# Performance work log

Hardware: AMD Instinct MI355X
Metric: run time of the kernel (lower is better)

Reference implementation:

```python
import jax, jax.numpy as jnp
import numpy as np

B, SQ, SK, D, DV = 8, 2048, 4096, 512, 256

def setup_inputs() -> dict:
    key = jax.random.key(0)
    k1, k2, k3, k4, k5 = jax.random.split(key, 5)
    X = jax.random.normal(k1, (B, SQ, D), dtype=jnp.float32)
    Y = jax.random.normal(k2, (SK, D), dtype=jnp.float32)
    Z = jax.random.normal(k3, (SK, D), dtype=jnp.float32)
    # Linear weights (torch stores [out, in]); scaled like default init
    W_k = jax.random.normal(k4, (D, D), dtype=jnp.float32) / np.sqrt(D)
    W_v = jax.random.normal(k5, (DV, D), dtype=jnp.float32) / np.sqrt(D)
    return {"X": X, "Y": Y, "Z": Z, "W_k": W_k, "W_v": W_v, "rate": 0}


def reference(X, Y, Z, W_k, W_v, rate):
    # key = W_k(Y).unsqueeze(0): [1, SK, D]; value = W_v(Z).unsqueeze(0): [1, SK, DV]
    key = (Y @ W_k.T)[None]
    value = (Z @ W_v.T)[None]
    # scores = X @ key^T / sqrt(d): [B, SQ, SK] (key batch dim broadcasts)
    scale = 1.0 / jnp.sqrt(jnp.asarray(X.shape[-1], dtype=X.dtype))
    scores = jnp.matmul(X, jnp.swapaxes(key, 1, 2)) * scale
    attn = jax.nn.softmax(scores, axis=-1)
    # dropout layers act as identity in eval mode
    out = jnp.matmul(attn, value)  # [B, SQ, DV]
    return out
```

## Files before the change

kernel.cpp:

```cpp
#include <hip/hip_runtime.h>
#include <hip/hip_bf16.h>

#define NB    8
#define SQN   2048
#define SKN   4096
#define DDIM  512
#define DVDIM 256
#define NROWS (NB*SQN)
#define NS    2
#define NJ    ((SKN/64)/NS)

typedef __attribute__((ext_vector_type(8))) short bf16x8;
typedef __attribute__((ext_vector_type(4))) short bf16x4;
typedef __attribute__((ext_vector_type(4))) float f32x4;

__device__ __forceinline__ short f2bf(float f) {
    unsigned u = __float_as_uint(f);
    return (short)((u + 0x7FFFu + ((u >> 16) & 1u)) >> 16);
}

__device__ __forceinline__ void gload_lds16(const void* g, void* l) {
    __builtin_amdgcn_global_load_lds(
        (const __attribute__((address_space(1))) unsigned int*)g,
        (__attribute__((address_space(3))) unsigned int*)l, 16, 0, 0);
}

__global__ __launch_bounds__(256, 2) void proj_gemms(
    const float* __restrict__ Y, const float* __restrict__ Z,
    const float* __restrict__ Wk, const float* __restrict__ Wv,
    unsigned short* __restrict__ keyb, unsigned short* __restrict__ vtb)
{
    __shared__ short sA[64*128];
    __shared__ short sB[64*128];
    const float *A, *Bm;
    unsigned short* C;
    int N, m0, n0;
    if (blockIdx.z == 0) {
        A = Y; Bm = Wk; C = keyb; N = DDIM;
        m0 = blockIdx.x * 64; n0 = blockIdx.y * 64;
    } else {
        int lin = blockIdx.x * 8 + blockIdx.y;
        if (lin >= 256) return;
        A = Wv; Bm = Z; C = vtb; N = SKN;
        m0 = (lin >> 6) * 64; n0 = (lin & 63) * 64;
    }
    const int tid  = threadIdx.x;
    const int wave = tid >> 6;
    const int lane = tid & 63;
    const int quad = lane >> 4;
    const int l15  = lane & 15;

    f32x4 acc[4];
    #pragma unroll
    for (int n = 0; n < 4; ++n) { acc[n][0]=0.f; acc[n][1]=0.f; acc[n][2]=0.f; acc[n][3]=0.f; }

    float4 ra[8], rb[8];
    #pragma unroll
    for (int it = 0; it < 8; ++it) {
        int f = it*1024 + tid*4, row = f >> 7, col = f & 127;
        ra[it] = *(const float4*)(A  + (size_t)(m0+row)*DDIM + col);
        rb[it] = *(const float4*)(Bm + (size_t)(n0+row)*DDIM + col);
    }

    for (int kc = 0; kc < DDIM; kc += 128) {
        __syncthreads();
        #pragma unroll
        for (int it = 0; it < 8; ++it) {
            int f = it*1024 + tid*4;
            bf16x4 a4; a4[0]=f2bf(ra[it].x); a4[1]=f2bf(ra[it].y); a4[2]=f2bf(ra[it].z); a4[3]=f2bf(ra[it].w);
            *(bf16x4*)(sA + f) = a4;
            bf16x4 b4; b4[0]=f2bf(rb[it].x); b4[1]=f2bf(rb[it].y); b4[2]=f2bf(rb[it].z); b4[3]=f2bf(rb[it].w);
            *(bf16x4*)(sB + f) = b4;
        }
        __syncthreads();
        if (kc + 128 < DDIM) {
            #pragma unroll
            for (int it = 0; it < 8; ++it) {
                int f = it*1024 + tid*4, row = f >> 7, col = f & 127;
                ra[it] = *(const float4*)(A  + (size_t)(m0+row)*DDIM + kc + 128 + col);
                rb[it] = *(const float4*)(Bm + (size_t)(n0+row)*DDIM + kc + 128 + col);
            }
        }
        #pragma unroll
        for (int t = 0; t < 4; ++t) {
            bf16x8 af = *(const bf16x8*)(sA + (wave*16 + l15)*128 + t*32 + quad*8);
            #pragma unroll
            for (int n = 0; n < 4; ++n) {
                bf16x8 bfr = *(const bf16x8*)(sB + (n*16 + l15)*128 + t*32 + quad*8);
                acc[n] = __builtin_amdgcn_mfma_f32_16x16x32_bf16(af, bfr, acc[n], 0, 0, 0);
            }
        }
    }
    #pragma unroll
    for (int n = 0; n < 4; ++n)
        #pragma unroll
        for (int r = 0; r < 4; ++r) {
            int m  = m0 + wave*16 + quad*4 + r;
            int nn = n0 + n*16 + l15;
            C[(size_t)m*N + nn] = (unsigned short)f2bf(acc[n][r]);
        }
}

__global__ __launch_bounds__(256, 2) void attn_fused(
    const float* __restrict__ X,
    const unsigned short* __restrict__ Kb,
    const unsigned short* __restrict__ Vt,
    float* __restrict__ Opart,
    float* __restrict__ Mpart,
    float* __restrict__ Lpart)
{
    __shared__ short sK[2][8192];
    __shared__ short sV[16384];
    __shared__ short sP[4096];
    const int tid  = threadIdx.x;
    const int wave = tid >> 6;
    const int lane = tid & 63;
    const int quad = lane >> 4;
    const int l15  = lane & 15;
    const int l7   = lane & 7;
    const int split = blockIdx.y;
    const int q0   = blockIdx.x * 64;
    const int sb0  = split * NJ;
    const float scale = 0.04419417382415922f;

    bf16x8 qf[16];
    {
        const float* xrow = X + (size_t)(q0 + wave*16 + l15) * DDIM;
        #pragma unroll
        for (int t = 0; t < 16; ++t) {
            float4 a = *(const float4*)(xrow + t*32 + quad*8);
            float4 b = *(const float4*)(xrow + t*32 + quad*8 + 4);
            bf16x8 q;
            q[0]=f2bf(a.x*scale); q[1]=f2bf(a.y*scale); q[2]=f2bf(a.z*scale); q[3]=f2bf(a.w*scale);
            q[4]=f2bf(b.x*scale); q[5]=f2bf(b.y*scale); q[6]=f2bf(b.z*scale); q[7]=f2bf(b.w*scale);
            qf[t] = q;
        }
    }

    f32x4 o[16];
    #pragma unroll
    for (int i = 0; i < 16; ++i) { o[i][0]=0.f; o[i][1]=0.f; o[i][2]=0.f; o[i][3]=0.f; }
    float m_r[4] = {-1e30f,-1e30f,-1e30f,-1e30f};
    float l_r[4] = {0.f,0.f,0.f,0.f};
    short* sPw = sP + wave*1024;

    const int wq   = wave*4 + quad;
    const int vrow = wave*8 + (lane>>3);
    const int vswz = (l7 ^ (lane>>3)) << 3;

    #define STAGE_K(sk0_, c_, buf_)                                            \
        do {                                                                   \
            const unsigned short* ksrc_ = Kb + (size_t)((sk0_) + wq)*DDIM      \
                + (c_)*128 + ((l15 ^ wq) << 3);                                \
            char* kdst_ = (char*)(buf_) + wave*1024;                           \
            _Pragma("unroll")                                                  \
            for (int it_ = 0; it_ < 4; ++it_)                                  \
                gload_lds16(ksrc_ + (size_t)it_*16*DDIM, kdst_ + it_*4096);    \
        } while (0)

    STAGE_K(sb0*64, 0, sK[0]);

    for (int j = 0; j < NJ; ++j) {
        const int sk0 = (sb0 + j) * 64;
        f32x4 s[4];
        #pragma unroll
        for (int n = 0; n < 4; ++n) { s[n][0]=0.f; s[n][1]=0.f; s[n][2]=0.f; s[n][3]=0.f; }

        #pragma unroll
        for (int c = 0; c < 4; ++c) {
            __syncthreads();
            if (c == 0) {
                const unsigned short* vsrc = Vt + sk0 + (size_t)vrow*SKN + vswz;
                char* vdst = (char*)sV + wave*1024;
                #pragma unroll
                for (int it = 0; it < 8; ++it)
                    gload_lds16(vsrc + (size_t)it*32*SKN, vdst + it*4096);
            }
            if (c < 3)            STAGE_K(sk0,      c + 1, sK[(c + 1) & 1]);
            else if (j + 1 < NJ)  STAGE_K(sk0 + 64, 0,     sK[0]);
            const short* sKc = sK[c & 1];
            #pragma unroll
            for (int t = 0; t < 4; ++t) {
                bf16x8 af = qf[c*4 + t];
                #pragma unroll
                for (int n = 0; n < 4; ++n) {
                    bf16x8 bfr = *(const bf16x8*)(sKc + (n*16 + l15)*128
                                                  + (((t*4 + quad) ^ l15) << 3));
                    s[n] = __builtin_amdgcn_mfma_f32_16x16x32_bf16(af, bfr, s[n], 0, 0, 0);
                }
            }
        }

        float alpha[4];
        int need_rescale = 0;
        #pragma unroll
        for (int r = 0; r < 4; ++r) {
            float v = fmaxf(fmaxf(s[0][r], s[1][r]), fmaxf(s[2][r], s[3][r]));
            v = fmaxf(v, __shfl_xor(v, 1));
            v = fmaxf(v, __shfl_xor(v, 2));
            v = fmaxf(v, __shfl_xor(v, 4));
            v = fmaxf(v, __shfl_xor(v, 8));
            float mn = fmaxf(m_r[r], v);
            float a  = __expf(m_r[r] - mn);
            alpha[r] = a;
            need_rescale |= (a < 1.0f);
            m_r[r] = mn;
            const int row = quad*4 + r;
            short* prow = sPw + row*64 + l7;
            const int rx = row & 7;
            float sum = 0.f;
            #pragma unroll
            for (int n = 0; n < 4; ++n) {
                float pv = __expf(s[n][r] - mn);
                sum += pv;
                prow[((n*2 + (l15 >> 3)) ^ rx) << 3] = f2bf(pv);
            }
            sum += __shfl_xor(sum, 1);
            sum += __shfl_xor(sum, 2);
            sum += __shfl_xor(sum, 4);
            sum += __shfl_xor(sum, 8);
            l_r[r] = l_r[r]*a + sum;
        }
        if (__any(need_rescale)) {
            #pragma unroll
            for (int n2 = 0; n2 < 16; ++n2)
                #pragma unroll
                for (int r = 0; r < 4; ++r) o[n2][r] *= alpha[r];
        }

        #pragma unroll
        for (int t2 = 0; t2 < 2; ++t2) {
            const int cx = (((t2*4 + quad) ^ l7) << 3);
            bf16x8 af = *(const bf16x8*)(sPw + l15*64 + cx);
            #pragma unroll
            for (int n2 = 0; n2 < 16; ++n2) {
                bf16x8 bfr = *(const bf16x8*)(sV + (n2*16 + l15)*64 + cx);
                o[n2] = __builtin_amdgcn_mfma_f32_16x16x32_bf16(af, bfr, o[n2], 0, 0, 0);
            }
        }
    }
    #undef STAGE_K

    const size_t base = (size_t)split * NROWS;
    #pragma unroll
    for (int r = 0; r < 4; ++r) {
        int row = q0 + wave*16 + quad*4 + r;
        if (l15 == 0) { Mpart[base + row] = m_r[r]; Lpart[base + row] = l_r[r]; }
        float* orow = Opart + (base + row) * (size_t)DVDIM;
        #pragma unroll
        for (int n2 = 0; n2 < 16; ++n2)
            orow[n2*16 + l15] = o[n2][r];
    }
}

__global__ void combine_splits(
    const float* __restrict__ Opart, const float* __restrict__ Mpart,
    const float* __restrict__ Lpart, float* __restrict__ out)
{
    const int row = blockIdx.x * 4 + (threadIdx.x >> 6);
    const int dv4 = (threadIdx.x & 63) * 4;
    float M = -1e30f;
    #pragma unroll
    for (int s = 0; s < NS; ++s) M = fmaxf(M, Mpart[(size_t)s*NROWS + row]);
    float denom = 0.f;
    float4 acc = make_float4(0.f, 0.f, 0.f, 0.f);
    #pragma unroll
    for (int s = 0; s < NS; ++s) {
        float w = __expf(Mpart[(size_t)s*NROWS + row] - M);
        denom += Lpart[(size_t)s*NROWS + row] * w;
        float4 ov = *(const float4*)(Opart + ((size_t)s*NROWS + row)*DVDIM + dv4);
        acc.x += ov.x*w; acc.y += ov.y*w; acc.z += ov.z*w; acc.w += ov.w*w;
    }
    float inv = 1.0f / denom;
    *(float4*)(out + (size_t)row*DVDIM + dv4)
        = make_float4(acc.x*inv, acc.y*inv, acc.z*inv, acc.w*inv);
}

extern "C" void kernel_launch(void* const* d_in, const int* in_sizes, int n_in,
                              void* d_out, int out_size, void* d_ws, size_t ws_size,
                              hipStream_t stream) {
    const float* X  = (const float*)d_in[0];
    const float* Y  = (const float*)d_in[1];
    const float* Z  = (const float*)d_in[2];
    const float* Wk = (const float*)d_in[3];
    const float* Wv = (const float*)d_in[4];
    float* out = (float*)d_out;

    char* ws = (char*)d_ws;
    unsigned short* keyb = (unsigned short*)ws;
    unsigned short* vtb  = (unsigned short*)(ws + (4u<<20));
    float* Opart = (float*)(ws + (6u<<20));
    float* Mpart = (float*)(ws + (6u<<20) + (size_t)NS*NROWS*DVDIM*4);
    float* Lpart = Mpart + (size_t)NS*NROWS;

    proj_gemms<<<dim3(64, 8, 2), dim3(256), 0, stream>>>(Y, Z, Wk, Wv, keyb, vtb);
    attn_fused<<<dim3(NROWS/64, NS), dim3(256), 0, stream>>>(
        X, keyb, vtb, Opart, Mpart, Lpart);
    combine_splits<<<dim3(NROWS/4), dim3(256), 0, stream>>>(Opart, Mpart, Lpart, out);
}
```

Baseline: 299.4 us.

## Fuse projections, attention and split combine into one persistent kernel with grid barrier

Merges the projection GEMMs, the split-K attention and the split combine into a single launch. The projection tiles are spread across all 512 blocks, then a global atomic barrier makes every block wait before attention starts. The split combine now runs in the second-arriving block of each pair, which reads its partner's partial results from a ticket and flag instead of a separate kernel. The change also drops the double-buffered K staging in favour of a single buffer with an extra barrier per chunk, and adds a memset launch. This trades launch gaps and one partial write/read for less K-load overlap and a grid-wide spin barrier that relies on all blocks being co-resident.

```diff
diff --git a/kernel.cpp b/kernel.cpp
--- a/kernel.cpp
+++ b/kernel.cpp
@@ -9,6 +9,7 @@
 #define NROWS (NB*SQN)
 #define NS    2
 #define NJ    ((SKN/64)/NS)
+#define NBLK  (256*NS)
 
 typedef __attribute__((ext_vector_type(8))) short bf16x8;
 typedef __attribute__((ext_vector_type(4))) short bf16x4;
@@ -25,103 +26,95 @@
         (__attribute__((address_space(3))) unsigned int*)l, 16, 0, 0);
 }
 
-__global__ __launch_bounds__(256, 2) void proj_gemms(
-    const float* __restrict__ Y, const float* __restrict__ Z,
-    const float* __restrict__ Wk, const float* __restrict__ Wv,
-    unsigned short* __restrict__ keyb, unsigned short* __restrict__ vtb)
-{
-    __shared__ short sA[64*128];
-    __shared__ short sB[64*128];
-    const float *A, *Bm;
-    unsigned short* C;
-    int N, m0, n0;
-    if (blockIdx.z == 0) {
-        A = Y; Bm = Wk; C = keyb; N = DDIM;
-        m0 = blockIdx.x * 64; n0 = blockIdx.y * 64;
-    } else {
-        int lin = blockIdx.x * 8 + blockIdx.y;
-        if (lin >= 256) return;
-        A = Wv; Bm = Z; C = vtb; N = SKN;
-        m0 = (lin >> 6) * 64; n0 = (lin & 63) * 64;
-    }
-    const int tid  = threadIdx.x;
-    const int wave = tid >> 6;
-    const int lane = tid & 63;
-    const int quad = lane >> 4;
-    const int l15  = lane & 15;
-
-    f32x4 acc[4];
-    #pragma unroll
-    for (int n = 0; n < 4; ++n) { acc[n][0]=0.f; acc[n][1]=0.f; acc[n][2]=0.f; acc[n][3]=0.f; }
-
-    float4 ra[8], rb[8];
-    #pragma unroll
-    for (int it = 0; it < 8; ++it) {
-        int f = it*1024 + tid*4, row = f >> 7, col = f & 127;
-        ra[it] = *(const float4*)(A  + (size_t)(m0+row)*DDIM + col);
-        rb[it] = *(const float4*)(Bm + (size_t)(n0+row)*DDIM + col);
-    }
-
-    for (int kc = 0; kc < DDIM; kc += 128) {
-        __syncthreads();
-        #pragma unroll
-        for (int it = 0; it < 8; ++it) {
-            int f = it*1024 + tid*4;
-            bf16x4 a4; a4[0]=f2bf(ra[it].x); a4[1]=f2bf(ra[it].y); a4[2]=f2bf(ra[it].z); a4[3]=f2bf(ra[it].w);
-            *(bf16x4*)(sA + f) = a4;
-            bf16x4 b4; b4[0]=f2bf(rb[it].x); b4[1]=f2bf(rb[it].y); b4[2]=f2bf(rb[it].z); b4[3]=f2bf(rb[it].w);
-            *(bf16x4*)(sB + f) = b4;
-        }
-        __syncthreads();
-        if (kc + 128 < DDIM) {
-            #pragma unroll
-            for (int it = 0; it < 8; ++it) {
-                int f = it*1024 + tid*4, row = f >> 7, col = f & 127;
-                ra[it] = *(const float4*)(A  + (size_t)(m0+row)*DDIM + kc + 128 + col);
-                rb[it] = *(const float4*)(Bm + (size_t)(n0+row)*DDIM + kc + 128 + col);
-            }
-        }
-        #pragma unroll
-        for (int t = 0; t < 4; ++t) {
-            bf16x8 af = *(const bf16x8*)(sA + (wave*16 + l15)*128 + t*32 + quad*8);
-            #pragma unroll
-            for (int n = 0; n < 4; ++n) {
-                bf16x8 bfr = *(const bf16x8*)(sB + (n*16 + l15)*128 + t*32 + quad*8);
-                acc[n] = __builtin_amdgcn_mfma_f32_16x16x32_bf16(af, bfr, acc[n], 0, 0, 0);
-            }
-        }
-    }
-    #pragma unroll
-    for (int n = 0; n < 4; ++n)
-        #pragma unroll
-        for (int r = 0; r < 4; ++r) {
-            int m  = m0 + wave*16 + quad*4 + r;
-            int nn = n0 + n*16 + l15;
-            C[(size_t)m*N + nn] = (unsigned short)f2bf(acc[n][r]);
-        }
-}
-
-__global__ __launch_bounds__(256, 2) void attn_fused(
+__global__ __launch_bounds__(256, 2) void attn_all(
     const float* __restrict__ X,
-    const unsigned short* __restrict__ Kb,
-    const unsigned short* __restrict__ Vt,
+    const float* __restrict__ Y,
+    const float* __restrict__ Z,
+    const float* __restrict__ Wk,
+    const float* __restrict__ Wv,
+    unsigned short* __restrict__ keyb,
+    unsigned short* __restrict__ vtb,
     float* __restrict__ Opart,
     float* __restrict__ Mpart,
-    float* __restrict__ Lpart)
+    float* __restrict__ Lpart,
+    int* __restrict__ sync,
+    float* __restrict__ out)
 {
-    __shared__ short sK[2][8192];
-    __shared__ short sV[16384];
-    __shared__ short sP[4096];
+    __shared__ char smem[57344];
+    short* sK = (short*)smem;
+    short* sV = (short*)(smem + 16384);
+    short* sP = (short*)(smem + 49152);
+    short* sA = (short*)smem;
+    short* sB = (short*)(smem + 16384);
+
     const int tid  = threadIdx.x;
     const int wave = tid >> 6;
     const int lane = tid & 63;
     const int quad = lane >> 4;
     const int l15  = lane & 15;
     const int l7   = lane & 7;
+    const int qb    = blockIdx.x;
     const int split = blockIdx.y;
-    const int q0   = blockIdx.x * 64;
-    const int sb0  = split * NJ;
+    const int bid   = split * 256 + qb;
+    const int q0    = qb * 64;
     const float scale = 0.04419417382415922f;
+
+    for (int t = bid; t < 768; t += NBLK) {
+        const float *A, *Bm;
+        unsigned short* C;
+        int N, m0, n0;
+        if (t < 512) { A = Y;  Bm = Wk; C = keyb; N = DDIM; m0 = (t >> 3) << 6; n0 = (t & 7) << 6; }
+        else { int tt = t - 512; A = Wv; Bm = Z; C = vtb; N = SKN; m0 = (tt >> 6) << 6; n0 = (tt & 63) << 6; }
+
+        f32x4 acc[4];
+        #pragma unroll
+        for (int n = 0; n < 4; ++n) { acc[n][0]=0.f; acc[n][1]=0.f; acc[n][2]=0.f; acc[n][3]=0.f; }
+        float4 ra[8], rb[8];
+        #pragma unroll
+        for (int it = 0; it < 8; ++it) {
+            int f = it*1024 + tid*4, row = f >> 7, col = f & 127;
+            ra[it] = *(const float4*)(A  + (size_t)(m0+row)*DDIM + col);
+            rb[it] = *(const float4*)(Bm + (size_t)(n0+row)*DDIM + col);
+        }
+        for (int kc = 0; kc < DDIM; kc += 128) {
+            __syncthreads();
+            #pragma unroll
+            for (int it = 0; it < 8; ++it) {
+                int f = it*1024 + tid*4;
+                bf16x4 a4; a4[0]=f2bf(ra[it].x); a4[1]=f2bf(ra[it].y); a4[2]=f2bf(ra[it].z); a4[3]=f2bf(ra[it].w);
+                *(bf16x4*)(sA + f) = a4;
+                bf16x4 b4; b4[0]=f2bf(rb[it].x); b4[1]=f2bf(rb[it].y); b4[2]=f2bf(rb[it].z); b4[3]=f2bf(rb[it].w);
+                *(bf16x4*)(sB + f) = b4;
+            }
+            __syncthreads();
+            if (kc + 128 < DDIM) {
+                #pragma unroll
+                for (int it = 0; it < 8; ++it) {
+                    int f = it*1024 + tid*4, row = f >> 7, col = f & 127;
+                    ra[it] = *(const float4*)(A  + (size_t)(m0+row)*DDIM + kc + 128 + col);
+                    rb[it] = *(const float4*)(Bm + (size_t)(n0+row)*DDIM + kc + 128 + col);
+                }
+            }
+            #pragma unroll
+            for (int tt2 = 0; tt2 < 4; ++tt2) {
+                bf16x8 af = *(const bf16x8*)(sA + (wave*16 + l15)*128 + tt2*32 + quad*8);
+                #pragma unroll
+                for (int n = 0; n < 4; ++n) {
+                    bf16x8 bfr = *(const bf16x8*)(sB + (n*16 + l15)*128 + tt2*32 + quad*8);
+                    acc[n] = __builtin_amdgcn_mfma_f32_16x16x32_bf16(af, bfr, acc[n], 0, 0, 0);
+                }
+            }
+        }
+        #pragma unroll
+        for (int n = 0; n < 4; ++n)
+            #pragma unroll
+            for (int r = 0; r < 4; ++r) {
+                int m  = m0 + wave*16 + quad*4 + r;
+                int nn = n0 + n*16 + l15;
+                C[(size_t)m*N + nn] = (unsigned short)f2bf(acc[n][r]);
+            }
+    }
+    __syncthreads();
 
     bf16x8 qf[16];
     {
@@ -137,6 +130,14 @@
         }
     }
 
+    if (tid == 0) {
+        __threadfence();
+        __hip_atomic_fetch_add(&sync[0], 1, __ATOMIC_ACQ_REL, __HIP_MEMORY_SCOPE_AGENT);
+        while (__hip_atomic_load(&sync[0], __ATOMIC_ACQUIRE, __HIP_MEMORY_SCOPE_AGENT) < NBLK)
+            __builtin_amdgcn_s_sleep(10);
+    }
+    __syncthreads();
+
     f32x4 o[16];
     #pragma unroll
     for (int i = 0; i < 16; ++i) { o[i][0]=0.f; o[i][1]=0.f; o[i][2]=0.f; o[i][3]=0.f; }
@@ -147,18 +148,7 @@
     const int wq   = wave*4 + quad;
     const int vrow = wave*8 + (lane>>3);
     const int vswz = (l7 ^ (lane>>3)) << 3;
-
-    #define STAGE_K(sk0_, c_, buf_)                                            \
-        do {                                                                   \
-            const unsigned short* ksrc_ = Kb + (size_t)((sk0_) + wq)*DDIM      \
-                + (c_)*128 + ((l15 ^ wq) << 3);                                \
-            char* kdst_ = (char*)(buf_) + wave*1024;                           \
-            _Pragma("unroll")                                                  \
-            for (int it_ = 0; it_ < 4; ++it_)                                  \
-                gload_lds16(ksrc_ + (size_t)it_*16*DDIM, kdst_ + it_*4096);    \
-        } while (0)
-
-    STAGE_K(sb0*64, 0, sK[0]);
+    const int sb0  = split * NJ;
 
     for (int j = 0; j < NJ; ++j) {
         const int sk0 = (sb0 + j) * 64;
@@ -170,21 +160,25 @@
         for (int c = 0; c < 4; ++c) {
             __syncthreads();
             if (c == 0) {
-                const unsigned short* vsrc = Vt + sk0 + (size_t)vrow*SKN + vswz;
+                const unsigned short* vsrc = vtb + sk0 + (size_t)vrow*SKN + vswz;
                 char* vdst = (char*)sV + wave*1024;
                 #pragma unroll
                 for (int it = 0; it < 8; ++it)
                     gload_lds16(vsrc + (size_t)it*32*SKN, vdst + it*4096);
             }
-            if (c < 3)            STAGE_K(sk0,      c + 1, sK[(c + 1) & 1]);
-            else if (j + 1 < NJ)  STAGE_K(sk0 + 64, 0,     sK[0]);
-            const short* sKc = sK[c & 1];
+            const unsigned short* ksrc = keyb + (size_t)(sk0 + wq)*DDIM
+                + c*128 + ((l15 ^ wq) << 3);
+            char* kdst = (char*)sK + wave*1024;
+            #pragma unroll
+            for (int it = 0; it < 4; ++it)
+                gload_lds16(ksrc + (size_t)it*16*DDIM, kdst + it*4096);
+            __syncthreads();
             #pragma unroll
             for (int t = 0; t < 4; ++t) {
                 bf16x8 af = qf[c*4 + t];
                 #pragma unroll
                 for (int n = 0; n < 4; ++n) {
-                    bf16x8 bfr = *(const bf16x8*)(sKc + (n*16 + l15)*128
+                    bf16x8 bfr = *(const bf16x8*)(sK + (n*16 + l15)*128
                                                   + (((t*4 + quad) ^ l15) << 3));
                     s[n] = __builtin_amdgcn_mfma_f32_16x16x32_bf16(af, bfr, s[n], 0, 0, 0);
                 }
@@ -239,41 +233,57 @@
             }
         }
     }
-    #undef STAGE_K
-
-    const size_t base = (size_t)split * NROWS;
-    #pragma unroll
-    for (int r = 0; r < 4; ++r) {
-        int row = q0 + wave*16 + quad*4 + r;
-        if (l15 == 0) { Mpart[base + row] = m_r[r]; Lpart[base + row] = l_r[r]; }
-        float* orow = Opart + (base + row) * (size_t)DVDIM;
-        #pragma unroll
-        for (int n2 = 0; n2 < 16; ++n2)
-            orow[n2*16 + l15] = o[n2][r];
-    }
-}
-
-__global__ void combine_splits(
-    const float* __restrict__ Opart, const float* __restrict__ Mpart,
-    const float* __restrict__ Lpart, float* __restrict__ out)
-{
-    const int row = blockIdx.x * 4 + (threadIdx.x >> 6);
-    const int dv4 = (threadIdx.x & 63) * 4;
-    float M = -1e30f;
-    #pragma unroll
-    for (int s = 0; s < NS; ++s) M = fmaxf(M, Mpart[(size_t)s*NROWS + row]);
-    float denom = 0.f;
-    float4 acc = make_float4(0.f, 0.f, 0.f, 0.f);
-    #pragma unroll
-    for (int s = 0; s < NS; ++s) {
-        float w = __expf(Mpart[(size_t)s*NROWS + row] - M);
-        denom += Lpart[(size_t)s*NROWS + row] * w;
-        float4 ov = *(const float4*)(Opart + ((size_t)s*NROWS + row)*DVDIM + dv4);
-        acc.x += ov.x*w; acc.y += ov.y*w; acc.z += ov.z*w; acc.w += ov.w*w;
-    }
-    float inv = 1.0f / denom;
-    *(float4*)(out + (size_t)row*DVDIM + dv4)
-        = make_float4(acc.x*inv, acc.y*inv, acc.z*inv, acc.w*inv);
+
+    __syncthreads();
+    int* s_flag = (int*)smem;
+    if (tid == 0)
+        s_flag[0] = __hip_atomic_fetch_add(&sync[1 + qb], 1, __ATOMIC_ACQ_REL,
+                                           __HIP_MEMORY_SCOPE_AGENT);
+    __syncthreads();
+    const int ticket = s_flag[0];
+
+    if (ticket == 0) {
+        #pragma unroll
+        for (int r = 0; r < 4; ++r) {
+            int row = q0 + wave*16 + quad*4 + r;
+            if (l15 == 0) {
+                Mpart[(size_t)split*NROWS + row] = m_r[r];
+                Lpart[(size_t)split*NROWS + row] = l_r[r];
+            }
+            float* orow = Opart + ((size_t)split*NROWS + row) * DVDIM;
+            #pragma unroll
+            for (int n2 = 0; n2 < 16; ++n2)
+                orow[n2*16 + l15] = o[n2][r];
+        }
+        __syncthreads();
+        if (tid == 0) {
+            __threadfence();
+            __hip_atomic_store(&sync[257 + qb], 1, __ATOMIC_RELEASE,
+                               __HIP_MEMORY_SCOPE_AGENT);
+        }
+    } else {
+        if (tid == 0) {
+            while (!__hip_atomic_load(&sync[257 + qb], __ATOMIC_ACQUIRE,
+                                      __HIP_MEMORY_SCOPE_AGENT))
+                __builtin_amdgcn_s_sleep(4);
+        }
+        __syncthreads();
+        const int os = 1 - split;
+        #pragma unroll
+        for (int r = 0; r < 4; ++r) {
+            int row = q0 + wave*16 + quad*4 + r;
+            float mp = Mpart[(size_t)os*NROWS + row];
+            float lp = Lpart[(size_t)os*NROWS + row];
+            float M  = fmaxf(m_r[r], mp);
+            float w0 = __expf(m_r[r] - M), w1 = __expf(mp - M);
+            float inv = 1.0f / (l_r[r]*w0 + lp*w1);
+            const float* prow = Opart + ((size_t)os*NROWS + row) * DVDIM;
+            float* orow = out + (size_t)row * DVDIM;
+            #pragma unroll
+            for (int n2 = 0; n2 < 16; ++n2)
+                orow[n2*16 + l15] = (o[n2][r]*w0 + prow[n2*16 + l15]*w1) * inv;
+        }
+    }
 }
 
 extern "C" void kernel_launch(void* const* d_in, const int* in_sizes, int n_in,
@@ -290,11 +300,11 @@
     unsigned short* keyb = (unsigned short*)ws;
     unsigned short* vtb  = (unsigned short*)(ws + (4u<<20));
     float* Opart = (float*)(ws + (6u<<20));
-    float* Mpart = (float*)(ws + (6u<<20) + (size_t)NS*NROWS*DVDIM*4);
-    float* Lpart = Mpart + (size_t)NS*NROWS;
-
-    proj_gemms<<<dim3(64, 8, 2), dim3(256), 0, stream>>>(Y, Z, Wk, Wv, keyb, vtb);
-    attn_fused<<<dim3(NROWS/64, NS), dim3(256), 0, stream>>>(
-        X, keyb, vtb, Opart, Mpart, Lpart);
-    combine_splits<<<dim3(NROWS/4), dim3(256), 0, stream>>>(Opart, Mpart, Lpart, out);
+    float* Mpart = (float*)(ws + (6u<<20) + (32u<<20));
+    float* Lpart = (float*)(ws + (6u<<20) + (32u<<20) + 131072u);
+    int*   sync  = (int*)  (ws + (6u<<20) + (32u<<20) + 262144u);
+
+    hipMemsetAsync(sync, 0, 4096, stream);
+    attn_all<<<dim3(256, NS), dim3(256), 0, stream>>>(
+        X, Y, Z, Wk, Wv, keyb, vtb, Opart, Mpart, Lpart, sync, out);
 }
```

New measurement: 384.4 us. 1.28x slower.
